# Optimization experiments

Hardware: AMD Instinct MI355X
Metric: run time of the kernel (lower is better)

The kernel has to match this reference:

```python
import jax, jax.numpy as jnp
import numpy as np

EPS = 1e-9
THRESHOLD = 0.5


def _spatial_entropy(feat, w1, b1, w2, b2):
    # feat: [B, C, H, W]
    p = jax.nn.sigmoid(feat)
    # faithful to source: log(p+eps) - (1-p)*log(1-p+eps)
    ent = jnp.log(p + EPS) - (1.0 - p) * jnp.log(1.0 - p + EPS)  # [B,C,H,W]
    pooled = feat.mean(axis=(2, 3))                               # [B,C]
    h = jax.nn.relu(pooled @ w1 + b1)                             # [B,64]
    cw = jax.nn.sigmoid(h @ w2 + b2)                              # [B,C]
    se = jnp.einsum('bchw,bc->bhw', ent, cw)                      # [B,H,W]
    # F.normalize(x, dim=(1,2)): L2-normalize jointly over H,W
    norm = jnp.sqrt(jnp.sum(se * se, axis=(1, 2), keepdims=True))
    return se / jnp.maximum(norm, 1e-12)


def _low_entropy_mask(entropy_map):
    # entropy_map: [B,H,W] -> mask [B,1,H,W]
    thr = entropy_map.mean(axis=(1, 2), keepdims=True) * THRESHOLD
    return (entropy_map < thr).astype(entropy_map.dtype)[:, None, :, :]


def setup_inputs() -> dict:
    key = jax.random.key(0)
    k1, k2, k3, k4 = jax.random.split(key, 4)
    B, C, H, W = 16, 256, 64, 64
    vis_feat = jax.random.normal(k1, (B, C, H, W), dtype=jnp.float32)
    text_feat = jax.random.normal(k2, (B, C, H, W), dtype=jnp.float32)
    # channel attention MLP params (Linear(256,64) -> Linear(64,256))
    w1 = jax.random.normal(k3, (256, 64), dtype=jnp.float32) * 0.0625
    b1 = jnp.zeros((64,), dtype=jnp.float32)
    w2 = jax.random.normal(k4, (64, 256), dtype=jnp.float32) * 0.125
    b2 = jnp.zeros((256,), dtype=jnp.float32)
    return {"vis_feat": vis_feat, "text_feat": text_feat,
            "w1": w1, "b1": b1, "w2": w2, "b2": b2}


def reference(vis_feat, text_feat, w1, b1, w2, b2):
    vis_entropy = _spatial_entropy(vis_feat, w1, b1, w2, b2)    # [B,H,W]
    text_entropy = _spatial_entropy(text_feat, w1, b1, w2, b2)  # [B,H,W]
    vis_low = _low_entropy_mask(vis_entropy)                     # [B,1,H,W]
    text_low = _low_entropy_mask(text_entropy)                   # [B,1,H,W]
    enhanced = vis_feat * vis_low + text_feat * text_low * (1.0 - vis_low)
    return enhanced, vis_entropy, text_entropy
```

## Files before the change

kernel.cpp:

```cpp
#include <hip/hip_runtime.h>
#include <math.h>

#define B 16
#define C 256
#define HW 4096
#define EPSE 1e-9f
#define NTHREADS 256
#define CCHUNK 16

typedef float nfloat4 __attribute__((ext_vector_type(4)));

__device__ __forceinline__ void nt_store4(float* p, float4 v) {
    nfloat4 nv = { v.x, v.y, v.z, v.w };
    __builtin_nontemporal_store(nv, (nfloat4*)p);
}

__device__ __forceinline__ float fast_rcp(float x) { return __builtin_amdgcn_rcpf(x); }

__device__ __forceinline__ float entf(float x) {
    float e  = __expf(-x);
    float p  = fast_rcp(1.f + e);
    float l1 = __logf(p + EPSE);
    float q  = 1.f - p;
    float l2 = __logf(q + EPSE);
    return fmaf(-q, l2, l1);
}

__global__ void k_pooled(const float* __restrict__ vis,
                         const float* __restrict__ txt,
                         float* __restrict__ pooled,
                         float* __restrict__ se) {
    int row = blockIdx.x;
    if (row < 128) {
        ((float4*)se)[row * NTHREADS + threadIdx.x] = make_float4(0.f, 0.f, 0.f, 0.f);
    }
    int f  = row >> 12;
    int bc = row & (B * C - 1);
    const float* src = (f == 0 ? vis : txt) + (size_t)bc * HW + threadIdx.x * 16;

    float4 a = *(const float4*)(src + 0);
    float4 b = *(const float4*)(src + 4);
    float4 c = *(const float4*)(src + 8);
    float4 d = *(const float4*)(src + 12);
    float s = (((a.x + a.y) + (a.z + a.w)) + ((b.x + b.y) + (b.z + b.w)))
            + (((c.x + c.y) + (c.z + c.w)) + ((d.x + d.y) + (d.z + d.w)));

    for (int off = 32; off > 0; off >>= 1) s += __shfl_down(s, off);
    __shared__ float sm[4];
    if ((threadIdx.x & 63) == 0) sm[threadIdx.x >> 6] = s;
    __syncthreads();
    if (threadIdx.x == 0)
        pooled[row] = (sm[0] + sm[1] + sm[2] + sm[3]) * (1.0f / HW);
}

__global__ void k_mlp(const float* __restrict__ pooled,
                      const float* __restrict__ w1, const float* __restrict__ b1,
                      const float* __restrict__ w2, const float* __restrict__ b2,
                      float* __restrict__ cw) {
    __shared__ float pl[B * C];
    __shared__ float h[B * 64];
    int f = blockIdx.x;
    const float* P = pooled + f * B * C;
    for (int i = threadIdx.x; i < B * C; i += NTHREADS) pl[i] = P[i];
    __syncthreads();
    for (int o = threadIdx.x; o < B * 64; o += NTHREADS) {
        int b = o >> 6, j = o & 63;
        float acc = b1[j];
        for (int c = 0; c < C; ++c) acc = fmaf(pl[b * C + c], w1[c * 64 + j], acc);
        h[o] = fmaxf(acc, 0.f);
    }
    __syncthreads();
    for (int o = threadIdx.x; o < B * C; o += NTHREADS) {
        int b = o >> 8, c2 = o & 255;
        float acc = b2[c2];
        for (int j = 0; j < 64; ++j) acc = fmaf(h[b * 64 + j], w2[j * 256 + c2], acc);
        cw[f * B * C + o] = fast_rcp(1.f + __expf(-acc));
    }
}

__global__ void __launch_bounds__(NTHREADS, 4)
k_se(const float* __restrict__ vis,
     const float* __restrict__ txt,
     const float* __restrict__ cw,
     float* __restrict__ se) {
    int bx   = blockIdx.x;
    int cc   = bx & 15;
    int tile = (bx >> 4) & 3;
    int b    = (bx >> 6) & 15;
    int f    = bx >> 10;
    const float* src = (f == 0 ? vis : txt)
                       + (size_t)b * C * HW + (size_t)cc * CCHUNK * HW
                       + tile * 1024 + threadIdx.x * 4;

    __shared__ float cwl[CCHUNK];
    if (threadIdx.x < CCHUNK)
        cwl[threadIdx.x] = cw[f * B * C + b * C + cc * CCHUNK + threadIdx.x];
    __syncthreads();

    float4 acc = make_float4(0.f, 0.f, 0.f, 0.f);
    #pragma unroll
    for (int g = 0; g < CCHUNK / 8; ++g) {
        float4 xs[8];
        #pragma unroll
        for (int j = 0; j < 8; ++j)
            xs[j] = *(const float4*)(src + (size_t)(g * 8 + j) * HW);
        #pragma unroll
        for (int j = 0; j < 8; ++j) {
            float w = cwl[g * 8 + j];
            acc.x = fmaf(entf(xs[j].x), w, acc.x);
            acc.y = fmaf(entf(xs[j].y), w, acc.y);
            acc.z = fmaf(entf(xs[j].z), w, acc.z);
            acc.w = fmaf(entf(xs[j].w), w, acc.w);
        }
    }
    float* dst = se + (f * B + b) * HW + tile * 1024 + threadIdx.x * 4;
    atomicAdd(dst + 0, acc.x);
    atomicAdd(dst + 1, acc.y);
    atomicAdd(dst + 2, acc.z);
    atomicAdd(dst + 3, acc.w);
}

__global__ void k_stats(const float* __restrict__ se,
                        float* __restrict__ inv_norm,
                        float* __restrict__ thr) {
    int fb = blockIdx.x;
    const float4* s4 = (const float4*)(se + fb * HW);
    float s = 0.f, ss = 0.f;
    #pragma unroll
    for (int i = threadIdx.x; i < HW / 4; i += NTHREADS) {
        float4 v = s4[i];
        s  += v.x + v.y + v.z + v.w;
        ss = fmaf(v.x, v.x, ss); ss = fmaf(v.y, v.y, ss);
        ss = fmaf(v.z, v.z, ss); ss = fmaf(v.w, v.w, ss);
    }
    for (int off = 32; off > 0; off >>= 1) {
        s  += __shfl_down(s, off);
        ss += __shfl_down(ss, off);
    }
    __shared__ float sm[8];
    if ((threadIdx.x & 63) == 0) {
        sm[(threadIdx.x >> 6) * 2]     = s;
        sm[(threadIdx.x >> 6) * 2 + 1] = ss;
    }
    __syncthreads();
    if (threadIdx.x == 0) {
        float st  = sm[0] + sm[2] + sm[4] + sm[6];
        float sst = sm[1] + sm[3] + sm[5] + sm[7];
        inv_norm[fb] = 1.f / fmaxf(sqrtf(sst), 1e-12f);
        thr[fb]      = 0.5f * (st * (1.0f / HW));
    }
}

__global__ void __launch_bounds__(NTHREADS, 4)
k_final(const float* __restrict__ vis,
        const float* __restrict__ txt,
        const float* __restrict__ se,
        const float* __restrict__ inv_norm,
        const float* __restrict__ thr,
        float* __restrict__ out_enh,
        float* __restrict__ out_ent_vis,
        float* __restrict__ out_ent_text) {
    int bx   = blockIdx.x;
    int cg   = bx & 15;
    int tile = (bx >> 4) & 3;
    int b    = bx >> 6;

    int hw   = tile * 1024 + threadIdx.x * 4;
    int mapi = b * HW + hw;

    float4 sv = *(const float4*)(se + mapi);
    float4 st = *(const float4*)(se + B * HW + mapi);
    float tv = thr[b], tt = thr[B + b];

    if (cg == 0) {
        float inv = inv_norm[b], int_ = inv_norm[B + b];
        float4 ov = make_float4(sv.x * inv, sv.y * inv, sv.z * inv, sv.w * inv);
        float4 ot = make_float4(st.x * int_, st.y * int_, st.z * int_, st.w * int_);
        nt_store4(out_ent_vis + mapi, ov);
        nt_store4(out_ent_text + mapi, ot);
    }

    int m0 = sv.x < tv ? 1 : (st.x < tt ? 2 : 0);
    int m1 = sv.y < tv ? 1 : (st.y < tt ? 2 : 0);
    int m2 = sv.z < tv ? 1 : (st.z < tt ? 2 : 0);
    int m3 = sv.w < tv ? 1 : (st.w < tt ? 2 : 0);

    size_t base = (size_t)b * C * HW + (size_t)cg * 16 * HW + hw;
    #pragma unroll
    for (int g = 0; g < 2; ++g) {
        float4 vv[8], tt4[8];
        #pragma unroll
        for (int c = 0; c < 8; ++c) {
            size_t idx = base + (size_t)(g * 8 + c) * HW;
            vv[c]  = *(const float4*)(vis + idx);
            tt4[c] = *(const float4*)(txt + idx);
        }
        #pragma unroll
        for (int c = 0; c < 8; ++c) {
            size_t idx = base + (size_t)(g * 8 + c) * HW;
            float4 o;
            o.x = (m0 == 1) ? vv[c].x : ((m0 == 2) ? tt4[c].x : 0.f);
            o.y = (m1 == 1) ? vv[c].y : ((m1 == 2) ? tt4[c].y : 0.f);
            o.z = (m2 == 1) ? vv[c].z : ((m2 == 2) ? tt4[c].z : 0.f);
            o.w = (m3 == 1) ? vv[c].w : ((m3 == 2) ? tt4[c].w : 0.f);
            nt_store4(out_enh + idx, o);
        }
    }
}

extern "C" void kernel_launch(void* const* d_in, const int* in_sizes, int n_in,
                              void* d_out, int out_size, void* d_ws, size_t ws_size,
                              hipStream_t stream) {
    const float* vis = (const float*)d_in[0];
    const float* txt = (const float*)d_in[1];
    const float* w1  = (const float*)d_in[2];
    const float* b1  = (const float*)d_in[3];
    const float* w2  = (const float*)d_in[4];
    const float* b2  = (const float*)d_in[5];

    float* out_enh      = (float*)d_out;
    float* out_ent_vis  = out_enh + (size_t)B * C * HW;
    float* out_ent_text = out_ent_vis + B * HW;

    float* ws       = (float*)d_ws;
    float* pooled   = ws;
    float* cw       = ws + 8192;
    float* se       = ws + 16384;
    float* inv_norm = ws + 147456;
    float* thr      = ws + 147488;

    k_pooled<<<8192, NTHREADS, 0, stream>>>(vis, txt, pooled, se);
    k_mlp   <<<2,    NTHREADS, 0, stream>>>(pooled, w1, b1, w2, b2, cw);
    k_se    <<<2048, NTHREADS, 0, stream>>>(vis, txt, cw, se);
    k_stats <<<32,   NTHREADS, 0, stream>>>(se, inv_norm, thr);
    k_final <<<1024, NTHREADS, 0, stream>>>(vis, txt, se, inv_norm, thr,
                                            out_enh, out_ent_vis, out_ent_text);
}
```

Before: 261.1 us.

## Fuse stats reduction into entropy kernel via last-block counter

Removes the separate k_stats launch. Each k_se block now increments a per-(feature,batch) counter after its atomic adds, and the last of the 64 contributing blocks computes the sum and sum of squares for that map. Also changes k_pooled's loads from contiguous 16-float chunks per thread to strided float4 loads for better coalescing. This saves one launch and its gap between kernels, at the cost of an extra atomic and barrier in every k_se block plus a serial tail in the last blocks.

```diff
diff --git a/kernel.cpp b/kernel.cpp
--- a/kernel.cpp
+++ b/kernel.cpp
@@ -29,19 +29,21 @@
 __global__ void k_pooled(const float* __restrict__ vis,
                          const float* __restrict__ txt,
                          float* __restrict__ pooled,
-                         float* __restrict__ se) {
+                         float* __restrict__ se,
+                         int* __restrict__ cnt) {
     int row = blockIdx.x;
     if (row < 128) {
         ((float4*)se)[row * NTHREADS + threadIdx.x] = make_float4(0.f, 0.f, 0.f, 0.f);
+        if (row == 0 && threadIdx.x < 2 * B) cnt[threadIdx.x] = 0;
     }
     int f  = row >> 12;
     int bc = row & (B * C - 1);
-    const float* src = (f == 0 ? vis : txt) + (size_t)bc * HW + threadIdx.x * 16;
+    const float* src = (f == 0 ? vis : txt) + (size_t)bc * HW + threadIdx.x * 4;
 
     float4 a = *(const float4*)(src + 0);
-    float4 b = *(const float4*)(src + 4);
-    float4 c = *(const float4*)(src + 8);
-    float4 d = *(const float4*)(src + 12);
+    float4 b = *(const float4*)(src + 1024);
+    float4 c = *(const float4*)(src + 2048);
+    float4 d = *(const float4*)(src + 3072);
     float s = (((a.x + a.y) + (a.z + a.w)) + ((b.x + b.y) + (b.z + b.w)))
             + (((c.x + c.y) + (c.z + c.w)) + ((d.x + d.y) + (d.z + d.w)));
 
@@ -82,7 +84,10 @@
 k_se(const float* __restrict__ vis,
      const float* __restrict__ txt,
      const float* __restrict__ cw,
-     float* __restrict__ se) {
+     float* __restrict__ se,
+     float* __restrict__ inv_norm,
+     float* __restrict__ thr,
+     int* __restrict__ cnt) {
     int bx   = blockIdx.x;
     int cc   = bx & 15;
     int tile = (bx >> 4) & 3;
@@ -113,41 +118,44 @@
             acc.w = fmaf(entf(xs[j].w), w, acc.w);
         }
     }
-    float* dst = se + (f * B + b) * HW + tile * 1024 + threadIdx.x * 4;
+    int fb = f * B + b;
+    float* dst = se + (size_t)fb * HW + tile * 1024 + threadIdx.x * 4;
     atomicAdd(dst + 0, acc.x);
     atomicAdd(dst + 1, acc.y);
     atomicAdd(dst + 2, acc.z);
     atomicAdd(dst + 3, acc.w);
-}
-
-__global__ void k_stats(const float* __restrict__ se,
-                        float* __restrict__ inv_norm,
-                        float* __restrict__ thr) {
-    int fb = blockIdx.x;
-    const float4* s4 = (const float4*)(se + fb * HW);
-    float s = 0.f, ss = 0.f;
-    #pragma unroll
-    for (int i = threadIdx.x; i < HW / 4; i += NTHREADS) {
-        float4 v = s4[i];
-        s  += v.x + v.y + v.z + v.w;
-        ss = fmaf(v.x, v.x, ss); ss = fmaf(v.y, v.y, ss);
-        ss = fmaf(v.z, v.z, ss); ss = fmaf(v.w, v.w, ss);
-    }
-    for (int off = 32; off > 0; off >>= 1) {
-        s  += __shfl_down(s, off);
-        ss += __shfl_down(ss, off);
-    }
-    __shared__ float sm[8];
-    if ((threadIdx.x & 63) == 0) {
-        sm[(threadIdx.x >> 6) * 2]     = s;
-        sm[(threadIdx.x >> 6) * 2 + 1] = ss;
-    }
-    __syncthreads();
-    if (threadIdx.x == 0) {
-        float st  = sm[0] + sm[2] + sm[4] + sm[6];
-        float sst = sm[1] + sm[3] + sm[5] + sm[7];
-        inv_norm[fb] = 1.f / fmaxf(sqrtf(sst), 1e-12f);
-        thr[fb]      = 0.5f * (st * (1.0f / HW));
+
+    __syncthreads();
+    __shared__ int lastflag;
+    if (threadIdx.x == 0)
+        lastflag = (atomicAdd(&cnt[fb], 1) == 63) ? 1 : 0;
+    __syncthreads();
+    if (lastflag) {
+        __threadfence();
+        const float4* s4 = (const float4*)(se + (size_t)fb * HW);
+        float s = 0.f, ss = 0.f;
+        for (int i = threadIdx.x; i < HW / 4; i += NTHREADS) {
+            float4 v = s4[i];
+            s  += v.x + v.y + v.z + v.w;
+            ss = fmaf(v.x, v.x, ss); ss = fmaf(v.y, v.y, ss);
+            ss = fmaf(v.z, v.z, ss); ss = fmaf(v.w, v.w, ss);
+        }
+        for (int off = 32; off > 0; off >>= 1) {
+            s  += __shfl_down(s, off);
+            ss += __shfl_down(ss, off);
+        }
+        __shared__ float sm[8];
+        if ((threadIdx.x & 63) == 0) {
+            sm[(threadIdx.x >> 6) * 2]     = s;
+            sm[(threadIdx.x >> 6) * 2 + 1] = ss;
+        }
+        __syncthreads();
+        if (threadIdx.x == 0) {
+            float st  = sm[0] + sm[2] + sm[4] + sm[6];
+            float sst = sm[1] + sm[3] + sm[5] + sm[7];
+            inv_norm[fb] = 1.f / fmaxf(sqrtf(sst), 1e-12f);
+            thr[fb]      = 0.5f * (st * (1.0f / HW));
+        }
     }
 }
 
@@ -228,11 +236,11 @@
     float* se       = ws + 16384;
     float* inv_norm = ws + 147456;
     float* thr      = ws + 147488;
-
-    k_pooled<<<8192, NTHREADS, 0, stream>>>(vis, txt, pooled, se);
+    int*   cnt      = (int*)(ws + 147520);
+
+    k_pooled<<<8192, NTHREADS, 0, stream>>>(vis, txt, pooled, se, cnt);
     k_mlp   <<<2,    NTHREADS, 0, stream>>>(pooled, w1, b1, w2, b2, cw);
-    k_se    <<<2048, NTHREADS, 0, stream>>>(vis, txt, cw, se);
-    k_stats <<<32,   NTHREADS, 0, stream>>>(se, inv_norm, thr);
+    k_se    <<<2048, NTHREADS, 0, stream>>>(vis, txt, cw, se, inv_norm, thr, cnt);
     k_final <<<1024, NTHREADS, 0, stream>>>(vis, txt, se, inv_norm, thr,
                                             out_enh, out_ent_vis, out_ent_text);
 }
```

New measurement: 287.1 us. 1.1x slower.

## Fuse MLP into entropy kernel and stats into final kernel, drop two launches

Applied to the files above, without the earlier changes.

The channel-attention MLP is recomputed redundantly in each k_se block, covering only the 16 channel weights that block needs. The per-map norm and threshold reduction is recomputed in every k_final block instead of running as a separate kernel. The pooling kernel now uses coalesced strided float4 loads. This removes two tiny, poorly parallel launches, especially the 2-block MLP kernel, at the cost of redundant MLP work and redundant reads of the se maps in every block.

```diff
diff --git a/kernel.cpp b/kernel.cpp
--- a/kernel.cpp
+++ b/kernel.cpp
@@ -31,17 +31,17 @@
                          float* __restrict__ pooled,
                          float* __restrict__ se) {
     int row = blockIdx.x;
-    if (row < 128) {
+    if (row < 128)
         ((float4*)se)[row * NTHREADS + threadIdx.x] = make_float4(0.f, 0.f, 0.f, 0.f);
-    }
+
     int f  = row >> 12;
     int bc = row & (B * C - 1);
-    const float* src = (f == 0 ? vis : txt) + (size_t)bc * HW + threadIdx.x * 16;
+    const float* src = (f == 0 ? vis : txt) + (size_t)bc * HW + threadIdx.x * 4;
 
     float4 a = *(const float4*)(src + 0);
-    float4 b = *(const float4*)(src + 4);
-    float4 c = *(const float4*)(src + 8);
-    float4 d = *(const float4*)(src + 12);
+    float4 b = *(const float4*)(src + 1024);
+    float4 c = *(const float4*)(src + 2048);
+    float4 d = *(const float4*)(src + 3072);
     float s = (((a.x + a.y) + (a.z + a.w)) + ((b.x + b.y) + (b.z + b.w)))
             + (((c.x + c.y) + (c.z + c.w)) + ((d.x + d.y) + (d.z + d.w)));
 
@@ -53,49 +53,49 @@
         pooled[row] = (sm[0] + sm[1] + sm[2] + sm[3]) * (1.0f / HW);
 }
 
-__global__ void k_mlp(const float* __restrict__ pooled,
-                      const float* __restrict__ w1, const float* __restrict__ b1,
-                      const float* __restrict__ w2, const float* __restrict__ b2,
-                      float* __restrict__ cw) {
-    __shared__ float pl[B * C];
-    __shared__ float h[B * 64];
-    int f = blockIdx.x;
-    const float* P = pooled + f * B * C;
-    for (int i = threadIdx.x; i < B * C; i += NTHREADS) pl[i] = P[i];
-    __syncthreads();
-    for (int o = threadIdx.x; o < B * 64; o += NTHREADS) {
-        int b = o >> 6, j = o & 63;
-        float acc = b1[j];
-        for (int c = 0; c < C; ++c) acc = fmaf(pl[b * C + c], w1[c * 64 + j], acc);
-        h[o] = fmaxf(acc, 0.f);
-    }
-    __syncthreads();
-    for (int o = threadIdx.x; o < B * C; o += NTHREADS) {
-        int b = o >> 8, c2 = o & 255;
-        float acc = b2[c2];
-        for (int j = 0; j < 64; ++j) acc = fmaf(h[b * 64 + j], w2[j * 256 + c2], acc);
-        cw[f * B * C + o] = fast_rcp(1.f + __expf(-acc));
-    }
-}
-
 __global__ void __launch_bounds__(NTHREADS, 4)
 k_se(const float* __restrict__ vis,
      const float* __restrict__ txt,
-     const float* __restrict__ cw,
+     const float* __restrict__ pooled,
+     const float* __restrict__ w1, const float* __restrict__ b1,
+     const float* __restrict__ w2, const float* __restrict__ b2,
      float* __restrict__ se) {
+    __shared__ float pl[C];
+    __shared__ float h[64];
+    __shared__ float cwl[CCHUNK];
+
+    const int tid  = threadIdx.x;
     int bx   = blockIdx.x;
     int cc   = bx & 15;
     int tile = (bx >> 4) & 3;
     int b    = (bx >> 6) & 15;
     int f    = bx >> 10;
+
+    pl[tid] = pooled[(f * B + b) * C + tid];
+    __syncthreads();
+
+    if (tid < 64) {
+        float acc = b1[tid];
+        const float* w1p = w1 + tid;
+        #pragma unroll 8
+        for (int c2 = 0; c2 < C; ++c2)
+            acc = fmaf(pl[c2], w1p[(size_t)c2 * 64], acc);
+        h[tid] = fmaxf(acc, 0.f);
+    }
+    __syncthreads();
+    if (tid < CCHUNK) {
+        int c2 = cc * CCHUNK + tid;
+        float acc = b2[c2];
+        #pragma unroll 8
+        for (int j = 0; j < 64; ++j)
+            acc = fmaf(h[j], w2[j * 256 + c2], acc);
+        cwl[tid] = fast_rcp(1.f + __expf(-acc));
+    }
+    __syncthreads();
+
     const float* src = (f == 0 ? vis : txt)
                        + (size_t)b * C * HW + (size_t)cc * CCHUNK * HW
-                       + tile * 1024 + threadIdx.x * 4;
-
-    __shared__ float cwl[CCHUNK];
-    if (threadIdx.x < CCHUNK)
-        cwl[threadIdx.x] = cw[f * B * C + b * C + cc * CCHUNK + threadIdx.x];
-    __syncthreads();
+                       + tile * 1024 + tid * 4;
 
     float4 acc = make_float4(0.f, 0.f, 0.f, 0.f);
     #pragma unroll
@@ -113,67 +113,76 @@
             acc.w = fmaf(entf(xs[j].w), w, acc.w);
         }
     }
-    float* dst = se + (f * B + b) * HW + tile * 1024 + threadIdx.x * 4;
+    float* dst = se + (size_t)(f * B + b) * HW + tile * 1024 + tid * 4;
     atomicAdd(dst + 0, acc.x);
     atomicAdd(dst + 1, acc.y);
     atomicAdd(dst + 2, acc.z);
     atomicAdd(dst + 3, acc.w);
 }
 
-__global__ void k_stats(const float* __restrict__ se,
-                        float* __restrict__ inv_norm,
-                        float* __restrict__ thr) {
-    int fb = blockIdx.x;
-    const float4* s4 = (const float4*)(se + fb * HW);
-    float s = 0.f, ss = 0.f;
-    #pragma unroll
-    for (int i = threadIdx.x; i < HW / 4; i += NTHREADS) {
-        float4 v = s4[i];
-        s  += v.x + v.y + v.z + v.w;
-        ss = fmaf(v.x, v.x, ss); ss = fmaf(v.y, v.y, ss);
-        ss = fmaf(v.z, v.z, ss); ss = fmaf(v.w, v.w, ss);
-    }
-    for (int off = 32; off > 0; off >>= 1) {
-        s  += __shfl_down(s, off);
-        ss += __shfl_down(ss, off);
-    }
-    __shared__ float sm[8];
-    if ((threadIdx.x & 63) == 0) {
-        sm[(threadIdx.x >> 6) * 2]     = s;
-        sm[(threadIdx.x >> 6) * 2 + 1] = ss;
-    }
-    __syncthreads();
-    if (threadIdx.x == 0) {
-        float st  = sm[0] + sm[2] + sm[4] + sm[6];
-        float sst = sm[1] + sm[3] + sm[5] + sm[7];
-        inv_norm[fb] = 1.f / fmaxf(sqrtf(sst), 1e-12f);
-        thr[fb]      = 0.5f * (st * (1.0f / HW));
-    }
-}
-
 __global__ void __launch_bounds__(NTHREADS, 4)
 k_final(const float* __restrict__ vis,
         const float* __restrict__ txt,
         const float* __restrict__ se,
-        const float* __restrict__ inv_norm,
-        const float* __restrict__ thr,
         float* __restrict__ out_enh,
         float* __restrict__ out_ent_vis,
         float* __restrict__ out_ent_text) {
+    const int tid = threadIdx.x;
     int bx   = blockIdx.x;
     int cg   = bx & 15;
     int tile = (bx >> 4) & 3;
     int b    = bx >> 6;
 
-    int hw   = tile * 1024 + threadIdx.x * 4;
+    const float4* s0 = (const float4*)(se + (size_t)b * HW);
+    const float4* s1 = (const float4*)(se + (size_t)(B + b) * HW);
+    float su0 = 0.f, sq0 = 0.f, su1 = 0.f, sq1 = 0.f;
+    #pragma unroll
+    for (int i = tid; i < HW / 4; i += NTHREADS) {
+        float4 v = s0[i];
+        su0 += v.x + v.y + v.z + v.w;
+        sq0 = fmaf(v.x, v.x, sq0); sq0 = fmaf(v.y, v.y, sq0);
+        sq0 = fmaf(v.z, v.z, sq0); sq0 = fmaf(v.w, v.w, sq0);
+        float4 w = s1[i];
+        su1 += w.x + w.y + w.z + w.w;
+        sq1 = fmaf(w.x, w.x, sq1); sq1 = fmaf(w.y, w.y, sq1);
+        sq1 = fmaf(w.z, w.z, sq1); sq1 = fmaf(w.w, w.w, sq1);
+    }
+    #pragma unroll
+    for (int off = 32; off > 0; off >>= 1) {
+        su0 += __shfl_down(su0, off);
+        sq0 += __shfl_down(sq0, off);
+        su1 += __shfl_down(su1, off);
+        sq1 += __shfl_down(sq1, off);
+    }
+    __shared__ float sred[16];
+    __shared__ float bcv[4];
+    if ((tid & 63) == 0) {
+        int w = tid >> 6;
+        sred[w * 4 + 0] = su0; sred[w * 4 + 1] = sq0;
+        sred[w * 4 + 2] = su1; sred[w * 4 + 3] = sq1;
+    }
+    __syncthreads();
+    if (tid == 0) {
+        float st0  = sred[0] + sred[4] + sred[8]  + sred[12];
+        float sst0 = sred[1] + sred[5] + sred[9]  + sred[13];
+        float st1  = sred[2] + sred[6] + sred[10] + sred[14];
+        float sst1 = sred[3] + sred[7] + sred[11] + sred[15];
+        bcv[0] = 0.5f * (st0 * (1.0f / HW));
+        bcv[1] = 0.5f * (st1 * (1.0f / HW));
+        bcv[2] = 1.f / fmaxf(sqrtf(sst0), 1e-12f);
+        bcv[3] = 1.f / fmaxf(sqrtf(sst1), 1e-12f);
+    }
+    __syncthreads();
+    float tv = bcv[0], tt = bcv[1];
+
+    int hw   = tile * 1024 + tid * 4;
     int mapi = b * HW + hw;
 
     float4 sv = *(const float4*)(se + mapi);
     float4 st = *(const float4*)(se + B * HW + mapi);
-    float tv = thr[b], tt = thr[B + b];
 
     if (cg == 0) {
-        float inv = inv_norm[b], int_ = inv_norm[B + b];
+        float inv = bcv[2], int_ = bcv[3];
         float4 ov = make_float4(sv.x * inv, sv.y * inv, sv.z * inv, sv.w * inv);
         float4 ot = make_float4(st.x * int_, st.y * int_, st.z * int_, st.w * int_);
         nt_store4(out_ent_vis + mapi, ov);
@@ -222,17 +231,13 @@
     float* out_ent_vis  = out_enh + (size_t)B * C * HW;
     float* out_ent_text = out_ent_vis + B * HW;
 
-    float* ws       = (float*)d_ws;
-    float* pooled   = ws;
-    float* cw       = ws + 8192;
-    float* se       = ws + 16384;
-    float* inv_norm = ws + 147456;
-    float* thr      = ws + 147488;
+    float* ws     = (float*)d_ws;
+    float* pooled = ws;
+    float* se     = ws + 8192;
 
     k_pooled<<<8192, NTHREADS, 0, stream>>>(vis, txt, pooled, se);
-    k_mlp   <<<2,    NTHREADS, 0, stream>>>(pooled, w1, b1, w2, b2, cw);
-    k_se    <<<2048, NTHREADS, 0, stream>>>(vis, txt, cw, se);
-    k_stats <<<32,   NTHREADS, 0, stream>>>(se, inv_norm, thr);
-    k_final <<<1024, NTHREADS, 0, stream>>>(vis, txt, se, inv_norm, thr,
+    k_se    <<<2048, NTHREADS, 0, stream>>>(vis, txt, pooled,
+                                            w1, b1, w2, b2, se);
+    k_final <<<1024, NTHREADS, 0, stream>>>(vis, txt, se,
                                             out_enh, out_ent_vis, out_ent_text);
 }
```

Measured after the change: 245.1 us. 1.07x faster.
